# Kernel tuning notes

Hardware: AMD Instinct MI355X
Metric: run time of the kernel (lower is better)

## Reference

```python
import jax, jax.numpy as jnp
import numpy as np

TAU = 1.0   # temperature
BETA = 1.0  # instance_alingment_weight


def setup_inputs() -> dict:
    key = jax.random.key(0)
    k1, k2, k3 = jax.random.split(key, 3)
    N, D = 1024, 128
    return {
        "x": jax.random.normal(k1, (N, D), dtype=jnp.float32),
        "aug_x": jax.random.normal(k2, (N, D), dtype=jnp.float32),
        "label_prompt_embedding": jax.random.normal(k3, (N, D), dtype=jnp.float32),
    }


def _pair_loss(x, y, scale):
    # positive distances: ||x_i - y_i|| / (tau * sqrt(D)), shape [N]
    pos = jnp.linalg.norm(x - y, axis=1) * scale
    # pairwise distance matrix [N, N] via broadcasted [N, N, D] diff (as original)
    dm = jnp.linalg.norm(x[:, None, :] - y[None, :, :], axis=-1) * scale
    denom = jnp.sum(jnp.exp(dm), axis=1)  # [N]
    # log(exp(pos) / denom) == pos - log(denom)
    return jnp.mean(pos - jnp.log(denom))


def reference(x, aug_x, label_prompt_embedding):
    D = x.shape[-1]
    scale = 1.0 / (TAU * np.sqrt(D).astype(np.float32))
    center_alignment_loss = _pair_loss(x, label_prompt_embedding, scale)
    instance_alignment_loss = _pair_loss(x, aug_x, scale)
    alignment_loss = center_alignment_loss + BETA * instance_alignment_loss
    return (alignment_loss, center_alignment_loss, instance_alignment_loss)
```

## Files before the change

kernel.cpp:

```cpp
#include <hip/hip_runtime.h>
#include <math.h>

#define NN 1024
#define DD 128

typedef __bf16 bf16x8 __attribute__((ext_vector_type(8)));
typedef float  floatx4 __attribute__((ext_vector_type(4)));

#define WS_NORMS  786432
#define WS_ACC    798720

__global__ __launch_bounds__(256) void align_prep(
    const float* __restrict__ x, const float* __restrict__ lp,
    const float* __restrict__ aug, __bf16* __restrict__ mats,
    float* __restrict__ norms, float* __restrict__ acc)
{
    if (blockIdx.x == 0 && threadIdx.x < 3) acc[threadIdx.x] = 0.0f;

    const int w    = threadIdx.x >> 6;
    const int lane = threadIdx.x & 63;
    const int gw   = blockIdx.x * 4 + w;
    const int a    = gw >> 10;
    const int r    = gw & 1023;
    const float* src = (a == 0 ? x : (a == 1 ? lp : aug)) + (size_t)r * DD + lane * 2;
    const float2 v = *(const float2*)src;
    float sq = v.x * v.x + v.y * v.y;
    union { __bf16 b[2]; unsigned u; } t;
    t.b[0] = (__bf16)v.x; t.b[1] = (__bf16)v.y;
    *(unsigned*)(mats + (size_t)a * (NN * DD) + (size_t)r * DD + lane * 2) = t.u;
#pragma unroll
    for (int m = 1; m < 64; m <<= 1) sq += __shfl_xor(sq, m);
    if (lane == 0) norms[a * NN + r] = sq;
}

__global__ __launch_bounds__(512) void align_pair_fused(
    const __bf16* __restrict__ mats, const float* __restrict__ norms,
    float* __restrict__ acc, float* __restrict__ out)
{
    const float SCALE = 0.08838834764831845f;
    const int bx = blockIdx.x;
    const int p  = blockIdx.y;
    const __bf16* __restrict__ A = mats;
    const __bf16* __restrict__ B = mats + (size_t)(p ? 2 : 1) * (NN * DD);
    const float*  __restrict__ nx = norms;
    const float*  __restrict__ ny = norms + (p ? 2 : 1) * NN;

    const int i0   = bx * 16;
    const int tid  = threadIdx.x;
    const int w    = tid >> 6;
    const int lane = tid & 63;
    const int col  = lane & 15;
    const int quad = lane >> 4;

    const __bf16* arow = A + (size_t)(i0 + col) * DD + quad * 8;
    bf16x8 afrag[4];
#pragma unroll
    for (int c = 0; c < 4; ++c) afrag[c] = *(const bf16x8*)(arow + c * 32);
    const float4 nxr = *(const float4*)(nx + i0 + quad * 4);

    float denom[4] = {0.f, 0.f, 0.f, 0.f};
    float pos[4]   = {0.f, 0.f, 0.f, 0.f};

#pragma unroll 2
    for (int jt = 0; jt < 8; ++jt) {
        const int j0 = jt * 128 + w * 16;
        const __bf16* brow = B + (size_t)(j0 + col) * DD + quad * 8;
        bf16x8 bfrag[4];
#pragma unroll
        for (int c = 0; c < 4; ++c) bfrag[c] = *(const bf16x8*)(brow + c * 32);
        const float nyv = ny[j0 + col];

        floatx4 acc4 = {0.f, 0.f, 0.f, 0.f};
#pragma unroll
        for (int c = 0; c < 4; ++c)
            acc4 = __builtin_amdgcn_mfma_f32_16x16x32_bf16(afrag[c], bfrag[c], acc4, 0, 0, 0);

#pragma unroll
        for (int r = 0; r < 4; ++r) {
            const int row = quad * 4 + r;
            float d2 = fmaf(-2.f, acc4[r], nxr[r] + nyv);
            d2 = fmaxf(d2, 0.f);
            const float dm = SCALE * sqrtf(d2);
            denom[r] += __expf(dm);
            if (j0 + col == i0 + row) pos[r] = dm;
        }
    }

#pragma unroll
    for (int r = 0; r < 4; ++r) {
#pragma unroll
        for (int m = 1; m < 16; m <<= 1) {
            denom[r] += __shfl_xor(denom[r], m);
            pos[r]   += __shfl_xor(pos[r], m);
        }
    }

    __shared__ float ld_den[8][16];
    __shared__ float ld_pos[8][16];
    if (col == 0) {
#pragma unroll
        for (int r = 0; r < 4; ++r) {
            ld_den[w][quad * 4 + r] = denom[r];
            ld_pos[w][quad * 4 + r] = pos[r];
        }
    }
    __syncthreads();

    float contrib = 0.f;
    if (tid < 16) {
        float den = 0.f, po = 0.f;
#pragma unroll
        for (int k = 0; k < 8; ++k) { den += ld_den[k][tid]; po += ld_pos[k][tid]; }
        contrib = po - __logf(den);
    }
    if (w == 0) {
#pragma unroll
        for (int m = 1; m < 16; m <<= 1) contrib += __shfl_xor(contrib, m);
    }
    if (tid == 0) {
        atomicAdd(&acc[p], contrib);
        __threadfence();
        const unsigned old = atomicAdd((unsigned*)(acc + 2), 1u);
        if (old == 127u) {
            const float a  = atomicAdd(&acc[0], 0.0f);
            const float b  = atomicAdd(&acc[1], 0.0f);
            const float inv = 1.0f / (float)NN;
            const float c  = a * inv;
            const float ia = b * inv;
            out[0] = c + ia;
            out[1] = c;
            out[2] = ia;
        }
    }
}

extern "C" void kernel_launch(void* const* d_in, const int* in_sizes, int n_in,
                              void* d_out, int out_size, void* d_ws, size_t ws_size,
                              hipStream_t stream) {
    const float* x   = (const float*)d_in[0];
    const float* aug = (const float*)d_in[1];
    const float* lp  = (const float*)d_in[2];
    float* out       = (float*)d_out;

    char* ws = (char*)d_ws;
    __bf16* mats  = (__bf16*)ws;
    float*  norms = (float*)(ws + WS_NORMS);
    float*  acc   = (float*)(ws + WS_ACC);

    align_prep<<<768, 256, 0, stream>>>(x, lp, aug, mats, norms, acc);
    align_pair_fused<<<dim3(64, 2), 512, 0, stream>>>(mats, norms, acc, out);
}
```

Baseline: 71.36 us.

## Split pairwise column range across blocks with atomic partial reductions

```diff
diff --git a/kernel.cpp b/kernel.cpp
--- a/kernel.cpp
+++ b/kernel.cpp
@@ -3,19 +3,28 @@
 
 #define NN 1024
 #define DD 128
+#define JCH 8
 
 typedef __bf16 bf16x8 __attribute__((ext_vector_type(8)));
 typedef float  floatx4 __attribute__((ext_vector_type(4)));
 
 #define WS_NORMS  786432
-#define WS_ACC    798720
+#define WS_DENOM  798720
+#define WS_POS    806912
+#define WS_ACC    815104
+#define WS_TCNT   815112
+#define WS_GCNT   815624
+#define ZERO_WORDS 4227
 
 __global__ __launch_bounds__(256) void align_prep(
     const float* __restrict__ x, const float* __restrict__ lp,
     const float* __restrict__ aug, __bf16* __restrict__ mats,
-    float* __restrict__ norms, float* __restrict__ acc)
+    float* __restrict__ norms, unsigned* __restrict__ zero_base)
 {
-    if (blockIdx.x == 0 && threadIdx.x < 3) acc[threadIdx.x] = 0.0f;
+    if (blockIdx.x < 17) {
+        const unsigned zi = blockIdx.x * 256 + threadIdx.x;
+        if (zi < ZERO_WORDS) zero_base[zi] = 0u;
+    }
 
     const int w    = threadIdx.x >> 6;
     const int lane = threadIdx.x & 63;
@@ -33,13 +42,16 @@
     if (lane == 0) norms[a * NN + r] = sq;
 }
 
-__global__ __launch_bounds__(512) void align_pair_fused(
+__global__ __launch_bounds__(256) void align_pair_kernel(
     const __bf16* __restrict__ mats, const float* __restrict__ norms,
-    float* __restrict__ acc, float* __restrict__ out)
+    float* __restrict__ denom, float* __restrict__ posb,
+    float* __restrict__ acc, unsigned* __restrict__ tcnt,
+    unsigned* __restrict__ gcnt, float* __restrict__ out)
 {
     const float SCALE = 0.08838834764831845f;
     const int bx = blockIdx.x;
     const int p  = blockIdx.y;
+    const int jc = blockIdx.z;
     const __bf16* __restrict__ A = mats;
     const __bf16* __restrict__ B = mats + (size_t)(p ? 2 : 1) * (NN * DD);
     const float*  __restrict__ nx = norms;
@@ -58,12 +70,12 @@
     for (int c = 0; c < 4; ++c) afrag[c] = *(const bf16x8*)(arow + c * 32);
     const float4 nxr = *(const float4*)(nx + i0 + quad * 4);
 
-    float denom[4] = {0.f, 0.f, 0.f, 0.f};
-    float pos[4]   = {0.f, 0.f, 0.f, 0.f};
+    float den4[4] = {0.f, 0.f, 0.f, 0.f};
+    float pos4[4] = {0.f, 0.f, 0.f, 0.f};
 
-#pragma unroll 2
-    for (int jt = 0; jt < 8; ++jt) {
-        const int j0 = jt * 128 + w * 16;
+#pragma unroll
+    for (int t = 0; t < 2; ++t) {
+        const int j0 = jc * 128 + t * 64 + w * 16;
         const __bf16* brow = B + (size_t)(j0 + col) * DD + quad * 8;
         bf16x8 bfrag[4];
 #pragma unroll
@@ -81,8 +93,8 @@
             float d2 = fmaf(-2.f, acc4[r], nxr[r] + nyv);
             d2 = fmaxf(d2, 0.f);
             const float dm = SCALE * sqrtf(d2);
-            denom[r] += __expf(dm);
-            if (j0 + col == i0 + row) pos[r] = dm;
+            den4[r] += __expf(dm);
+            if (j0 + col == i0 + row) pos4[r] = dm;
         }
     }
 
@@ -90,28 +102,44 @@
     for (int r = 0; r < 4; ++r) {
 #pragma unroll
         for (int m = 1; m < 16; m <<= 1) {
-            denom[r] += __shfl_xor(denom[r], m);
-            pos[r]   += __shfl_xor(pos[r], m);
+            den4[r] += __shfl_xor(den4[r], m);
+            pos4[r] += __shfl_xor(pos4[r], m);
         }
     }
 
-    __shared__ float ld_den[8][16];
-    __shared__ float ld_pos[8][16];
+    __shared__ float ld_den[4][16];
+    __shared__ float ld_pos[4][16];
     if (col == 0) {
 #pragma unroll
         for (int r = 0; r < 4; ++r) {
-            ld_den[w][quad * 4 + r] = denom[r];
-            ld_pos[w][quad * 4 + r] = pos[r];
+            ld_den[w][quad * 4 + r] = den4[r];
+            ld_pos[w][quad * 4 + r] = pos4[r];
         }
     }
     __syncthreads();
 
+    const bool hasdiag = (jc == (bx >> 3));
+    if (tid < 16) {
+        const float den = ld_den[0][tid] + ld_den[1][tid] + ld_den[2][tid] + ld_den[3][tid];
+        atomicAdd(&denom[p * NN + i0 + tid], den);
+        if (hasdiag) {
+            const float po = ld_pos[0][tid] + ld_pos[1][tid] + ld_pos[2][tid] + ld_pos[3][tid];
+            atomicAdd(&posb[p * NN + i0 + tid], po);
+        }
+    }
+    __threadfence();
+    __syncthreads();
+
+    __shared__ unsigned fin;
+    if (tid == 0) fin = (atomicAdd(&tcnt[p * 64 + bx], 1u) == JCH - 1) ? 1u : 0u;
+    __syncthreads();
+    if (!fin) return;
+
     float contrib = 0.f;
     if (tid < 16) {
-        float den = 0.f, po = 0.f;
-#pragma unroll
-        for (int k = 0; k < 8; ++k) { den += ld_den[k][tid]; po += ld_pos[k][tid]; }
-        contrib = po - __logf(den);
+        const float dsum = atomicAdd(&denom[p * NN + i0 + tid], 0.0f);
+        const float psum = atomicAdd(&posb[p * NN + i0 + tid], 0.0f);
+        contrib = psum - __logf(dsum);
     }
     if (w == 0) {
 #pragma unroll
@@ -120,8 +148,7 @@
     if (tid == 0) {
         atomicAdd(&acc[p], contrib);
         __threadfence();
-        const unsigned old = atomicAdd((unsigned*)(acc + 2), 1u);
-        if (old == 127u) {
+        if (atomicAdd(gcnt, 1u) == 127u) {
             const float a  = atomicAdd(&acc[0], 0.0f);
             const float b  = atomicAdd(&acc[1], 0.0f);
             const float inv = 1.0f / (float)NN;
@@ -143,10 +170,15 @@
     float* out       = (float*)d_out;
 
     char* ws = (char*)d_ws;
-    __bf16* mats  = (__bf16*)ws;
-    float*  norms = (float*)(ws + WS_NORMS);
-    float*  acc   = (float*)(ws + WS_ACC);
+    __bf16*   mats  = (__bf16*)ws;
+    float*    norms = (float*)(ws + WS_NORMS);
+    float*    denom = (float*)(ws + WS_DENOM);
+    float*    posb  = (float*)(ws + WS_POS);
+    float*    acc   = (float*)(ws + WS_ACC);
+    unsigned* tcnt  = (unsigned*)(ws + WS_TCNT);
+    unsigned* gcnt  = (unsigned*)(ws + WS_GCNT);
 
-    align_prep<<<768, 256, 0, stream>>>(x, lp, aug, mats, norms, acc);
-    align_pair_fused<<<dim3(64, 2), 512, 0, stream>>>(mats, norms, acc, out);
+    align_prep<<<768, 256, 0, stream>>>(x, lp, aug, mats, norms, (unsigned*)(ws + WS_DENOM));
+    align_pair_kernel<<<dim3(64, 2, JCH), 256, 0, stream>>>(
+        mats, norms, denom, posb, acc, tcnt, gcnt, out);
 }
```

Measured after the change: 127.8 us. 79.2% more time.
